# Optimization experiments

Measured on AMD Instinct MI355X. Metric: run time of the kernel, lower is better.

## Reference

```python
import jax, jax.numpy as jnp
import numpy as np

NUM_COMPONENTS = 4
HEADS = 16


def setup_inputs() -> dict:
    key = jax.random.key(0)
    ks = jax.random.split(key, 7)
    BC, S, D = 8, 4096, 1024      # batch_times_comp = batch(2) * num_components(4)
    Se, De = 256, 2048            # encoder seq len, encoder hidden dim
    sc = 0.02                     # keep linear outputs in a sane range
    return {
        "hidden_states": jax.random.normal(ks[0], (BC, S, D), jnp.float32),
        "encoder_hidden_states": jax.random.normal(ks[1], (BC, Se, De), jnp.float32),
        "Wq": jax.random.normal(ks[2], (D, D), jnp.float32) * sc,
        "Wk": jax.random.normal(ks[3], (De, D), jnp.float32) * sc,
        "Wv": jax.random.normal(ks[4], (De, D), jnp.float32) * sc,
        "Wo": jax.random.normal(ks[5], (D, D), jnp.float32) * sc,
        "bo": jnp.zeros((D,), jnp.float32),
    }


def reference(hidden_states, encoder_hidden_states, Wq, Wk, Wv, Wo, bo):
    C, H = NUM_COMPONENTS, HEADS
    BC, S, D = hidden_states.shape
    Se = encoder_hidden_states.shape[1]
    B = BC // C
    dh = D // H
    scale = dh ** -0.5  # attn.scale (learn_temperature=False)

    # projections -> [BC, H, S(e), dh]
    q = (hidden_states @ Wq).reshape(BC, S, H, dh).transpose(0, 2, 1, 3)
    k = (encoder_hidden_states @ Wk).reshape(BC, Se, H, dh).transpose(0, 2, 1, 3)
    v = (encoder_hidden_states @ Wv).reshape(BC, Se, H, dh).transpose(0, 2, 1, 3)

    # dense scores [BC, H, S, Se]
    scores = jnp.einsum("bhsd,bhtd->bhst", q, k) * scale
    # softmax over the COMPONENT axis (dim 0 after the 5D view)
    scores5 = scores.reshape(C, B, H, S, Se)
    w = jax.nn.softmax(scores5, axis=0)  # [C, B, H, S, Se]

    # compositional (negative) entropy, summed over components -> [B, H, S, Se]
    compositional_entropy = (w * jnp.log(w)).sum(axis=0)

    # rescale and attend
    w = (w * (C / Se)).reshape(BC, H, S, Se)
    out = jnp.einsum("bhst,bhtd->bhsd", w, v)
    out = out.transpose(0, 2, 1, 3).reshape(BC, S, D)

    # to_out[0] linear (+bias), to_out[1] dropout = identity at eval,
    # residual connection, rescale_output_factor = 1
    out = out @ Wo + bo + hidden_states
    return out, compositional_entropy
```

## Files before the change

### kernel.cpp

```cpp
#include <hip/hip_runtime.h>

typedef unsigned short u16;
typedef __bf16 bf16x4 __attribute__((ext_vector_type(4)));
typedef __bf16 bf16x8 __attribute__((ext_vector_type(8)));
typedef float f32x4 __attribute__((ext_vector_type(4)));
typedef u16 u16x4 __attribute__((ext_vector_type(4)));
typedef u16 u16x8 __attribute__((ext_vector_type(8)));

#define AS1P(p) ((__attribute__((address_space(1))) void*)(unsigned long long)(p))
#define AS3P(p) ((__attribute__((address_space(3))) void*)(unsigned long long)(p))
#define MFMA16(a, b, c) __builtin_amdgcn_mfma_f32_16x16x32_bf16((a), (b), (c), 0, 0, 0)

__device__ __forceinline__ u16 f2b(float x) { return __builtin_bit_cast(u16, (__bf16)x); }
__device__ __forceinline__ float b2f(u16 u) {
  return __builtin_bit_cast(float, (unsigned)u << 16);
}

__global__ __launch_bounds__(256) void cvt_f32_bf16(const float* __restrict__ in,
                                                    u16* __restrict__ out, int n4) {
  int stride = gridDim.x * blockDim.x;
  for (int i = blockIdx.x * blockDim.x + threadIdx.x; i < n4; i += stride) {
    f32x4 v = *(const f32x4*)(in + (long)i * 4);
    u16x4 o;
    o[0] = f2b(v[0]); o[1] = f2b(v[1]); o[2] = f2b(v[2]); o[3] = f2b(v[3]);
    *(u16x4*)(out + (long)i * 4) = o;
  }
}

__global__ __launch_bounds__(256) void wtrans(const float* __restrict__ W,
                                              u16* __restrict__ Wt, int K, int N) {
  __shared__ float tile[32][33];
  int nbk = K >> 5;
  int bk = blockIdx.x % nbk;
  int bn = blockIdx.x / nbk;
  int tx = threadIdx.x & 31, ty = threadIdx.x >> 5;
#pragma unroll
  for (int i = 0; i < 32; i += 8)
    tile[ty + i][tx] = W[(long)(bk * 32 + ty + i) * N + bn * 32 + tx];
  __syncthreads();
#pragma unroll
  for (int i = 0; i < 32; i += 8)
    Wt[(long)(bn * 32 + ty + i) * K + bk * 32 + tx] = f2b(tile[tx][ty + i]);
}

__global__ __launch_bounds__(256) void vtrans(const u16* __restrict__ kvb,
                                              u16* __restrict__ vt) {
  __shared__ u16 tile[32][33];
  int bt = blockIdx.x & 7;
  int bd = (blockIdx.x >> 3) & 31;
  int bc = blockIdx.x >> 8;
  int tx = threadIdx.x & 31, ty = threadIdx.x >> 5;
  const long ob = (long)bc * 1024 * 256;
  const float RS = 1.0f / 64.0f;
#pragma unroll
  for (int i = 0; i < 32; i += 8)
    tile[ty + i][tx] =
        kvb[((long)bc * 256 + bt * 32 + ty + i) * 2048 + 1024 + bd * 32 + tx];
  __syncthreads();
#pragma unroll
  for (int i = 0; i < 32; i += 8)
    vt[ob + (long)(bd * 32 + ty + i) * 256 + bt * 32 + tx] =
        f2b(b2f(tile[tx][ty + i]) * RS);
}

__global__ __launch_bounds__(256) void kfrag_build(const u16* __restrict__ kvb,
                                                   u16* __restrict__ kfrag) {
  int wv = ((int)blockIdx.x << 2) + (threadIdx.x >> 6);
  int lane = threadIdx.x & 63, lr = lane & 15, lg = lane >> 4;
  int ks = wv & 1, tsl = (wv >> 1) & 1, c = (wv >> 2) & 3;
  int ch = (wv >> 4) & 7, h = (wv >> 7) & 15, b = (wv >> 11) & 1;
  const u16* src = kvb + ((long)(c * 2 + b) * 256 + ch * 32 + tsl * 16 + lr) * 2048 +
                   h * 64 + ks * 32 + lg * 8;
  *(bf16x8*)(kfrag + (long)wv * 512 + lane * 8) = *(const bf16x8*)src;
}

__global__ __launch_bounds__(256) void vfrag_build(const u16* __restrict__ vtb,
                                                   u16* __restrict__ vfrag) {
  int wv = ((int)blockIdx.x << 2) + (threadIdx.x >> 6);
  int lane = threadIdx.x & 63, lr = lane & 15, lg = lane >> 4;
  int dsu = wv & 3, c = (wv >> 2) & 3;
  int ch = (wv >> 4) & 7, h = (wv >> 7) & 15, b = (wv >> 11) & 1;
  const u16* src = vtb + ((long)(c * 2 + b) * 1024 + h * 64 + dsu * 16 + lr) * 256 +
                   ch * 32 + lg * 8;
  *(bf16x8*)(vfrag + (long)wv * 512 + lane * 8) = *(const bf16x8*)src;
}

__global__ __launch_bounds__(256) void gemm_bt(
    const u16* __restrict__ A, const u16* __restrict__ Bt,
    u16* __restrict__ outb, int M, int N, int K, float ascale) {
  __shared__ u16 lA[128 * 64];
  __shared__ u16 lB[128 * 64];
  const int tid = threadIdx.x;
  const int lane = tid & 63;
  const int wid = tid >> 6;
  const int wm = wid >> 1, wn = wid & 1;
  const int lr = lane & 15, lg = lane >> 4;

  int bid = (int)blockIdx.x;
  int nwg = (int)gridDim.x;
  if ((nwg & 7) == 0) bid = (bid & 7) * (nwg >> 3) + (bid >> 3);

  const int nbn = N >> 7;
  const int bm = bid / nbn;
  const int bn = bid % nbn;
  const long arow0 = (long)bm * 128;
  const long brow0 = (long)bn * 128;

  f32x4 acc[4][4] = {};

  const int srow = tid >> 3;
  const int scol = tid & 7;

  for (int k0 = 0; k0 < K; k0 += 64) {
#pragma unroll
    for (int i = 0; i < 4; ++i) {
      int row = i * 32 + srow;
      int kc = scol ^ (row & 7);
      __builtin_amdgcn_global_load_lds(AS1P(A + (arow0 + row) * K + k0 + kc * 8),
                                       AS3P(lA + i * 2048 + (tid & ~63) * 8), 16, 0, 0);
    }
#pragma unroll
    for (int i = 0; i < 4; ++i) {
      int row = i * 32 + srow;
      int kc = scol ^ (row & 7);
      __builtin_amdgcn_global_load_lds(AS1P(Bt + (brow0 + row) * K + k0 + kc * 8),
                                       AS3P(lB + i * 2048 + (tid & ~63) * 8), 16, 0, 0);
    }
    asm volatile("s_waitcnt vmcnt(0)" ::: "memory");
    __syncthreads();

#pragma unroll
    for (int ks = 0; ks < 2; ++ks) {
      bf16x8 af[4], bfr[4];
#pragma unroll
      for (int m = 0; m < 4; ++m) {
        int row = wm * 64 + m * 16 + lr;
        int off = row * 128 + ks * 64 + lg * 16;
        off ^= (row & 7) << 4;
        af[m] = *(const bf16x8*)((const char*)lA + off);
      }
#pragma unroll
      for (int n = 0; n < 4; ++n) {
        int row = wn * 64 + n * 16 + lr;
        int off = row * 128 + ks * 64 + lg * 16;
        off ^= (row & 7) << 4;
        bfr[n] = *(const bf16x8*)((const char*)lB + off);
      }
#pragma unroll
      for (int m = 0; m < 4; ++m)
#pragma unroll
        for (int n = 0; n < 4; ++n)
          acc[m][n] = MFMA16(af[m], bfr[n], acc[m][n]);
    }
    __syncthreads();
  }

#pragma unroll
  for (int m = 0; m < 4; ++m)
#pragma unroll
    for (int n = 0; n < 4; ++n) {
      long col = brow0 + wn * 64 + n * 16 + lr;
#pragma unroll
      for (int r = 0; r < 4; ++r) {
        long row = arow0 + wm * 64 + m * 16 + lg * 4 + r;
        outb[row * N + col] = f2b(acc[m][n][r] * ascale);
      }
    }
}

template <int MODE>
__global__ __launch_bounds__(512, 2) void gemm256(
    const u16* __restrict__ A, const u16* __restrict__ Bt,
    u16* __restrict__ outb, float* __restrict__ outf,
    const float* __restrict__ bias, const u16* __restrict__ residb,
    int M, int N, int K, float ascale) {
  __shared__ u16 lds[2][2][256 * 64];
  const int tid = threadIdx.x;
  const int lane = tid & 63;
  const int wid = tid >> 6;
  const int wm = wid >> 2;
  const int wn = wid & 3;
  const int lr = lane & 15, lg = lane >> 4;

  int bid = (int)blockIdx.x;
  int nwg = (int)gridDim.x;
  bid = (bid & 7) * (nwg >> 3) + (bid >> 3);

  const int nbn = N >> 8;
  const int bm = bid / nbn;
  const int bn = bid % nbn;
  const long arow0 = (long)bm * 256;
  const long brow0 = (long)bn * 256;

  f32x4 acc[8][4] = {};

  const int srow = tid >> 3;
  const int scol = tid & 7;
  const int nt = K >> 6;

#define STAGE256(bf, t)                                                                \
  do {                                                                                 \
    int k0_ = (t) << 6;                                                                \
    _Pragma("unroll") for (int i = 0; i < 4; ++i) {                                    \
      int row = i * 64 + srow;                                                         \
      int kc = scol ^ (row & 7);                                                       \
      __builtin_amdgcn_global_load_lds(AS1P(A + (arow0 + row) * K + k0_ + kc * 8),     \
                                       AS3P(&lds[bf][0][0] + i * 4096 + (tid & ~63) * 8), \
                                       16, 0, 0);                                      \
    }                                                                                  \
    _Pragma("unroll") for (int i = 0; i < 4; ++i) {                                    \
      int row = i * 64 + srow;                                                         \
      int kc = scol ^ (row & 7);                                                       \
      __builtin_amdgcn_global_load_lds(AS1P(Bt + (brow0 + row) * K + k0_ + kc * 8),    \
                                       AS3P(&lds[bf][1][0] + i * 4096 + (tid & ~63) * 8), \
                                       16, 0, 0);                                      \
    }                                                                                  \
  } while (0)

#define COMPUTE256(bf)                                                                 \
  do {                                                                                 \
    _Pragma("unroll") for (int ks = 0; ks < 2; ++ks) {                                 \
      bf16x8 af[8], bfr[4];                                                            \
      _Pragma("unroll") for (int m = 0; m < 8; ++m) {                                  \
        int row = wm * 128 + m * 16 + lr;                                              \
        int off = row * 128 + ks * 64 + lg * 16;                                       \
        off ^= (row & 7) << 4;                                                         \
        af[m] = *(const bf16x8*)((const char*)&lds[bf][0][0] + off);                   \
      }                                                                                \
      _Pragma("unroll") for (int n = 0; n < 4; ++n) {                                  \
        int row = wn * 64 + n * 16 + lr;                                               \
        int off = row * 128 + ks * 64 + lg * 16;                                       \
        off ^= (row & 7) << 4;                                                         \
        bfr[n] = *(const bf16x8*)((const char*)&lds[bf][1][0] + off);                  \
      }                                                                                \
      _Pragma("unroll") for (int m = 0; m < 8; ++m)                                    \
          _Pragma("unroll") for (int n = 0; n < 4; ++n)                                \
              acc[m][n] = MFMA16(af[m], bfr[n], acc[m][n]);                            \
    }                                                                                  \
  } while (0)

  STAGE256(0, 0);
  asm volatile("s_waitcnt vmcnt(0)" ::: "memory");
  __syncthreads();
  int cur = 0;
  for (int t = 0; t < nt - 1; ++t) {
    STAGE256(cur ^ 1, t + 1);
    COMPUTE256(cur);
    asm volatile("s_waitcnt vmcnt(0)" ::: "memory");
    __syncthreads();
    cur ^= 1;
  }
  COMPUTE256(cur);

#pragma unroll
  for (int m = 0; m < 8; ++m)
#pragma unroll
    for (int n = 0; n < 4; ++n) {
      long col = brow0 + wn * 64 + n * 16 + lr;
#pragma unroll
      for (int r = 0; r < 4; ++r) {
        long row = arow0 + wm * 128 + m * 16 + lg * 4 + r;
        float v = acc[m][n][r];
        if (MODE == 1) {
          long idx = row * N + col;
          __builtin_nontemporal_store(v + bias[col] + b2f(residb[idx]), outf + idx);
        } else {
          outb[row * N + col] = f2b(v * ascale);
        }
      }
    }
#undef STAGE256
#undef COMPUTE256
}

__global__ __launch_bounds__(256, 1) void attn_fused(
    const u16* q,
    const u16* __restrict__ kfrag,
    const u16* __restrict__ vfrag,
    u16* attnout,
    float* __restrict__ ent) {
  const int B = 2, H = 16, S = 4096, Se = 256, D = 1024;
  __shared__ u16 ldsP[4 * 2304];
  const int tid = threadIdx.x;
  const int lane = tid & 63, wid = tid >> 6;
  const int lr = lane & 15, lg = lane >> 4;
  int bid = (int)blockIdx.x;
  bid = (bid & 7) * 256 + (bid >> 3);
  const int sblk = bid & 63;
  const int h = (bid >> 6) & 15;
  const int b = bid >> 10;
  const int s0 = sblk * 64 + wid * 16;

  u16* Pw = ldsP + wid * 2304;

  bf16x8 qf[4][2];
#pragma unroll
  for (int c = 0; c < 4; ++c)
#pragma unroll
    for (int ks = 0; ks < 2; ++ks)
      qf[c][ks] = *(const bf16x8*)(q + ((c * B + b) * (long)S + s0 + lr) * D +
                                   h * 64 + ks * 32 + lg * 8);

  const u16* kbh = kfrag + (long)(b * 16 + h) * 65536 + lane * 8;
  const u16* vbh = vfrag + (long)(b * 16 + h) * 65536 + lane * 8;
  float* entp = ent + ((long)(b * H + h) * S + s0 + lg * 4) * Se + lr;

  const float LN2 = 0.69314718056f;

  f32x4 oacc[4][4] = {};

  bf16x8 kf[16];
#pragma unroll
  for (int i = 0; i < 16; ++i) kf[i] = *(const bf16x8*)(kbh + (i << 9));

#pragma unroll
  for (int ch = 0; ch < 8; ++ch) {
    const u16* vc = vbh + ch * 8192;
    bf16x8 vf[16];
#pragma unroll
    for (int i = 0; i < 16; ++i) vf[i] = *(const bf16x8*)(vc + (i << 9));
    bf16x8 kfn[16];
    if (ch < 7) {
      const u16* kn = kbh + (ch + 1) * 8192;
#pragma unroll
      for (int i = 0; i < 16; ++i) kfn[i] = *(const bf16x8*)(kn + (i << 9));
    }
    __builtin_amdgcn_sched_barrier(0);

    f32x4 sacc[4][2] = {};
#pragma unroll
    for (int c = 0; c < 4; ++c)
#pragma unroll
      for (int tsl = 0; tsl < 2; ++tsl)
#pragma unroll
        for (int ks = 0; ks < 2; ++ks)
          sacc[c][tsl] = MFMA16(qf[c][ks], kf[c * 4 + tsl * 2 + ks], sacc[c][tsl]);

#pragma unroll
    for (int tsl = 0; tsl < 2; ++tsl) {
#pragma unroll
      for (int r = 0; r < 4; ++r) {
        float t0 = sacc[0][tsl][r];
        float t1 = sacc[1][tsl][r];
        float t2 = sacc[2][tsl][r];
        float t3 = sacc[3][tsl][r];
        float e0 = __builtin_amdgcn_exp2f(t0);
        float e1 = __builtin_amdgcn_exp2f(t1);
        float e2 = __builtin_amdgcn_exp2f(t2);
        float e3 = __builtin_amdgcn_exp2f(t3);
        float sum = (e0 + e1) + (e2 + e3);
        float inv = __builtin_amdgcn_rcpf(sum);
        float l2s = __builtin_amdgcn_logf(sum);
        float w0 = e0 * inv, w1 = e1 * inv, w2 = e2 * inv, w3 = e3 * inv;
        float entv = (w0 * t0 + w1 * t1 + w2 * t2 + w3 * t3 - l2s) * LN2;
        __builtin_nontemporal_store(entv, entp + r * Se + ch * 32 + tsl * 16);
        int pof = (lg * 4 + r) * 36 + tsl * 16 + lr;
        Pw[0 * 576 + pof] = f2b(w0);
        Pw[1 * 576 + pof] = f2b(w1);
        Pw[2 * 576 + pof] = f2b(w2);
        Pw[3 * 576 + pof] = f2b(w3);
      }
    }

#pragma unroll
    for (int c = 0; c < 4; ++c) {
      union { bf16x4 hh[2]; bf16x8 v; } pu;
      pu.hh[0] = *(const bf16x4*)(Pw + c * 576 + lr * 36 + lg * 8);
      pu.hh[1] = *(const bf16x4*)(Pw + c * 576 + lr * 36 + lg * 8 + 4);
      bf16x8 pf = pu.v;
#pragma unroll
      for (int dsu = 0; dsu < 4; ++dsu)
        oacc[c][dsu] = MFMA16(pf, vf[c * 4 + dsu], oacc[c][dsu]);
    }

    if (ch < 7) {
#pragma unroll
      for (int i = 0; i < 16; ++i) kf[i] = kfn[i];
    }
  }

#pragma unroll
  for (int c = 0; c < 4; ++c)
#pragma unroll
    for (int dsu = 0; dsu < 4; ++dsu)
#pragma unroll
      for (int r = 0; r < 4; ++r) {
        int s = s0 + lg * 4 + r;
        attnout[((c * B + b) * (long)S + s) * D + h * 64 + dsu * 16 + lr] =
            f2b(oacc[c][dsu][r]);
      }
}

extern "C" void kernel_launch(void* const* d_in, const int* in_sizes, int n_in,
                              void* d_out, int out_size, void* d_ws, size_t ws_size,
                              hipStream_t stream) {
  const float* hs  = (const float*)d_in[0];
  const float* ehs = (const float*)d_in[1];
  const float* Wq  = (const float*)d_in[2];
  const float* Wk  = (const float*)d_in[3];
  const float* Wv  = (const float*)d_in[4];
  const float* Wo  = (const float*)d_in[5];
  const float* bo  = (const float*)d_in[6];
  float* out = (float*)d_out;
  float* ent = out + (size_t)8 * 4096 * 1024;

  char* ws = (char*)d_ws;
  u16* hsb   = (u16*)(ws);
  u16* ehsb  = (u16*)(ws + 67108864);
  u16* kfrag = (u16*)(ws + 67108864);
  u16* vfrag = (u16*)(ws + 71303168);
  u16* wqT   = (u16*)(ws + 75497472);
  u16* wkT   = (u16*)(ws + 77594624);
  u16* wvT   = (u16*)(ws + 81788928);
  u16* woT   = (u16*)(ws + 85983232);
  u16* qb    = (u16*)(ws + 88080384);
  u16* kvb   = (u16*)(ws + 155189248);
  u16* vtb   = (u16*)(ws + 163577856);

  const float QSCALE = 0.125f * 1.44269504f;

  cvt_f32_bf16<<<2048, 256, 0, stream>>>(hs, hsb, (8 * 4096 * 1024) / 4);
  cvt_f32_bf16<<<512, 256, 0, stream>>>(ehs, ehsb, (8 * 256 * 2048) / 4);
  wtrans<<<1024, 256, 0, stream>>>(Wq, wqT, 1024, 1024);
  wtrans<<<2048, 256, 0, stream>>>(Wk, wkT, 2048, 1024);
  wtrans<<<2048, 256, 0, stream>>>(Wv, wvT, 2048, 1024);
  wtrans<<<1024, 256, 0, stream>>>(Wo, woT, 1024, 1024);
  gemm256<0><<<(32768 / 256) * (1024 / 256), 512, 0, stream>>>(
      hsb, wqT, qb, nullptr, nullptr, nullptr, 32768, 1024, 1024, QSCALE);
  gemm_bt<<<(2048 / 128) * (2048 / 128), 256, 0, stream>>>(
      ehsb, wkT, kvb, 2048, 2048, 2048, 1.0f);
  vtrans<<<2048, 256, 0, stream>>>(kvb, vtb);
  kfrag_build<<<1024, 256, 0, stream>>>(kvb, kfrag);
  vfrag_build<<<1024, 256, 0, stream>>>(vtb, vfrag);
  attn_fused<<<2048, 256, 0, stream>>>(qb, kfrag, vfrag, qb, ent);
  gemm256<1><<<(32768 / 256) * (1024 / 256), 512, 0, stream>>>(
      qb, woT, nullptr, out, bo, hsb, 32768, 1024, 1024, 1.0f);
}
```

Baseline: 394.7 us.

## Stage K/V fragments in LDS with double buffering and double rows per wave

The attention kernel now stages K and V fragments for each 32-key chunk into a double-buffered LDS region using direct global-to-LDS loads shared by all four waves, instead of each wave loading them into registers from global memory. Each wave also handles 32 query rows instead of 16, so every K/V fragment read from LDS feeds two MFMAs, and the grid is halved. This cuts redundant global K/V traffic and register pressure from the prefetch, at the cost of more LDS, a block barrier per chunk, and fewer blocks in flight.

```diff
diff --git a/kernel.cpp b/kernel.cpp
--- a/kernel.cpp
+++ b/kernel.cpp
@@ -280,103 +280,123 @@
     u16* attnout,
     float* __restrict__ ent) {
   const int B = 2, H = 16, S = 4096, Se = 256, D = 1024;
-  __shared__ u16 ldsP[4 * 2304];
+  __shared__ u16 kvs[2][32 * 512];
+  __shared__ u16 ldsP[4 * 4608];
   const int tid = threadIdx.x;
   const int lane = tid & 63, wid = tid >> 6;
   const int lr = lane & 15, lg = lane >> 4;
   int bid = (int)blockIdx.x;
-  bid = (bid & 7) * 256 + (bid >> 3);
-  const int sblk = bid & 63;
-  const int h = (bid >> 6) & 15;
-  const int b = bid >> 10;
-  const int s0 = sblk * 64 + wid * 16;
-
-  u16* Pw = ldsP + wid * 2304;
-
-  bf16x8 qf[4][2];
+  bid = (bid & 7) * 128 + (bid >> 3);
+  const int sblk = bid & 31;
+  const int h = (bid >> 5) & 15;
+  const int b = bid >> 9;
+  const int s0 = sblk * 128 + wid * 32;
+
+  u16* Pw = ldsP + wid * 4608;
+
+  bf16x8 qf[4][2][2];
 #pragma unroll
   for (int c = 0; c < 4; ++c)
 #pragma unroll
-    for (int ks = 0; ks < 2; ++ks)
-      qf[c][ks] = *(const bf16x8*)(q + ((c * B + b) * (long)S + s0 + lr) * D +
-                                   h * 64 + ks * 32 + lg * 8);
-
-  const u16* kbh = kfrag + (long)(b * 16 + h) * 65536 + lane * 8;
-  const u16* vbh = vfrag + (long)(b * 16 + h) * 65536 + lane * 8;
+    for (int st = 0; st < 2; ++st)
+#pragma unroll
+      for (int ks = 0; ks < 2; ++ks)
+        qf[c][st][ks] =
+            *(const bf16x8*)(q + ((c * B + b) * (long)S + s0 + st * 16 + lr) * D +
+                             h * 64 + ks * 32 + lg * 8);
+
+  const u16* kbh = kfrag + (long)(b * 16 + h) * 65536;
+  const u16* vbh = vfrag + (long)(b * 16 + h) * 65536;
   float* entp = ent + ((long)(b * H + h) * S + s0 + lg * 4) * Se + lr;
 
   const float LN2 = 0.69314718056f;
-
-  f32x4 oacc[4][4] = {};
-
-  bf16x8 kf[16];
-#pragma unroll
-  for (int i = 0; i < 16; ++i) kf[i] = *(const bf16x8*)(kbh + (i << 9));
+  const int g0 = wid * 8;
+
+  f32x4 oacc[4][4][2] = {};
+
+#define STAGEKV(buf, ch)                                                               \
+  do {                                                                                 \
+    _Pragma("unroll") for (int j = 0; j < 8; ++j) {                                    \
+      int f = g0 + j;                                                                  \
+      const u16* src = (f < 16 ? kbh + (ch) * 8192 + f * 512                           \
+                               : vbh + (ch) * 8192 + (f - 16) * 512) +                 \
+                       lane * 8;                                                       \
+      __builtin_amdgcn_global_load_lds(AS1P(src), AS3P(&kvs[buf][f * 512]), 16, 0, 0); \
+    }                                                                                  \
+  } while (0)
+
+  STAGEKV(0, 0);
+  __syncthreads();
 
 #pragma unroll
   for (int ch = 0; ch < 8; ++ch) {
-    const u16* vc = vbh + ch * 8192;
-    bf16x8 vf[16];
-#pragma unroll
-    for (int i = 0; i < 16; ++i) vf[i] = *(const bf16x8*)(vc + (i << 9));
-    bf16x8 kfn[16];
-    if (ch < 7) {
-      const u16* kn = kbh + (ch + 1) * 8192;
-#pragma unroll
-      for (int i = 0; i < 16; ++i) kfn[i] = *(const bf16x8*)(kn + (i << 9));
-    }
-    __builtin_amdgcn_sched_barrier(0);
-
-    f32x4 sacc[4][2] = {};
+    const int cur = ch & 1;
+    if (ch < 7) STAGEKV(cur ^ 1, ch + 1);
+    const u16* KV = kvs[cur];
+
+    f32x4 sacc[2][4][2] = {};
 #pragma unroll
     for (int c = 0; c < 4; ++c)
 #pragma unroll
       for (int tsl = 0; tsl < 2; ++tsl)
 #pragma unroll
-        for (int ks = 0; ks < 2; ++ks)
-          sacc[c][tsl] = MFMA16(qf[c][ks], kf[c * 4 + tsl * 2 + ks], sacc[c][tsl]);
-
-#pragma unroll
-    for (int tsl = 0; tsl < 2; ++tsl) {
-#pragma unroll
-      for (int r = 0; r < 4; ++r) {
-        float t0 = sacc[0][tsl][r];
-        float t1 = sacc[1][tsl][r];
-        float t2 = sacc[2][tsl][r];
-        float t3 = sacc[3][tsl][r];
-        float e0 = __builtin_amdgcn_exp2f(t0);
-        float e1 = __builtin_amdgcn_exp2f(t1);
-        float e2 = __builtin_amdgcn_exp2f(t2);
-        float e3 = __builtin_amdgcn_exp2f(t3);
-        float sum = (e0 + e1) + (e2 + e3);
-        float inv = __builtin_amdgcn_rcpf(sum);
-        float l2s = __builtin_amdgcn_logf(sum);
-        float w0 = e0 * inv, w1 = e1 * inv, w2 = e2 * inv, w3 = e3 * inv;
-        float entv = (w0 * t0 + w1 * t1 + w2 * t2 + w3 * t3 - l2s) * LN2;
-        __builtin_nontemporal_store(entv, entp + r * Se + ch * 32 + tsl * 16);
-        int pof = (lg * 4 + r) * 36 + tsl * 16 + lr;
-        Pw[0 * 576 + pof] = f2b(w0);
-        Pw[1 * 576 + pof] = f2b(w1);
-        Pw[2 * 576 + pof] = f2b(w2);
-        Pw[3 * 576 + pof] = f2b(w3);
+        for (int ks = 0; ks < 2; ++ks) {
+          bf16x8 kfv = *(const bf16x8*)(KV + (c * 4 + tsl * 2 + ks) * 512 + lane * 8);
+#pragma unroll
+          for (int st = 0; st < 2; ++st)
+            sacc[st][c][tsl] = MFMA16(qf[c][st][ks], kfv, sacc[st][c][tsl]);
+        }
+
+#pragma unroll
+    for (int st = 0; st < 2; ++st) {
+#pragma unroll
+      for (int tsl = 0; tsl < 2; ++tsl) {
+#pragma unroll
+        for (int r = 0; r < 4; ++r) {
+          float t0 = sacc[st][0][tsl][r];
+          float t1 = sacc[st][1][tsl][r];
+          float t2 = sacc[st][2][tsl][r];
+          float t3 = sacc[st][3][tsl][r];
+          float e0 = __builtin_amdgcn_exp2f(t0);
+          float e1 = __builtin_amdgcn_exp2f(t1);
+          float e2 = __builtin_amdgcn_exp2f(t2);
+          float e3 = __builtin_amdgcn_exp2f(t3);
+          float sum = (e0 + e1) + (e2 + e3);
+          float inv = __builtin_amdgcn_rcpf(sum);
+          float l2s = __builtin_amdgcn_logf(sum);
+          float w0 = e0 * inv, w1 = e1 * inv, w2 = e2 * inv, w3 = e3 * inv;
+          float entv = (w0 * t0 + w1 * t1 + w2 * t2 + w3 * t3 - l2s) * LN2;
+          __builtin_nontemporal_store(
+              entv, entp + (st * 16 + r) * Se + ch * 32 + tsl * 16);
+          int prow = st * 16 + lg * 4 + r;
+          int pof = prow * 36 + tsl * 16 + lr;
+          Pw[0 * 1152 + pof] = f2b(w0);
+          Pw[1 * 1152 + pof] = f2b(w1);
+          Pw[2 * 1152 + pof] = f2b(w2);
+          Pw[3 * 1152 + pof] = f2b(w3);
+        }
       }
     }
 
 #pragma unroll
     for (int c = 0; c < 4; ++c) {
-      union { bf16x4 hh[2]; bf16x8 v; } pu;
-      pu.hh[0] = *(const bf16x4*)(Pw + c * 576 + lr * 36 + lg * 8);
-      pu.hh[1] = *(const bf16x4*)(Pw + c * 576 + lr * 36 + lg * 8 + 4);
-      bf16x8 pf = pu.v;
-#pragma unroll
-      for (int dsu = 0; dsu < 4; ++dsu)
-        oacc[c][dsu] = MFMA16(pf, vf[c * 4 + dsu], oacc[c][dsu]);
-    }
-
-    if (ch < 7) {
-#pragma unroll
-      for (int i = 0; i < 16; ++i) kf[i] = kfn[i];
-    }
+      bf16x8 pf[2];
+#pragma unroll
+      for (int st = 0; st < 2; ++st) {
+        union { bf16x4 hh[2]; bf16x8 v; } pu;
+        pu.hh[0] = *(const bf16x4*)(Pw + c * 1152 + (st * 16 + lr) * 36 + lg * 8);
+        pu.hh[1] = *(const bf16x4*)(Pw + c * 1152 + (st * 16 + lr) * 36 + lg * 8 + 4);
+        pf[st] = pu.v;
+      }
+#pragma unroll
+      for (int dsu = 0; dsu < 4; ++dsu) {
+        bf16x8 vfv = *(const bf16x8*)(KV + (16 + c * 4 + dsu) * 512 + lane * 8);
+        oacc[c][dsu][0] = MFMA16(pf[0], vfv, oacc[c][dsu][0]);
+        oacc[c][dsu][1] = MFMA16(pf[1], vfv, oacc[c][dsu][1]);
+      }
+    }
+
+    __syncthreads();
   }
 
 #pragma unroll
@@ -384,11 +404,14 @@
 #pragma unroll
     for (int dsu = 0; dsu < 4; ++dsu)
 #pragma unroll
-      for (int r = 0; r < 4; ++r) {
-        int s = s0 + lg * 4 + r;
-        attnout[((c * B + b) * (long)S + s) * D + h * 64 + dsu * 16 + lr] =
-            f2b(oacc[c][dsu][r]);
-      }
+      for (int st = 0; st < 2; ++st)
+#pragma unroll
+        for (int r = 0; r < 4; ++r) {
+          long s = s0 + st * 16 + lg * 4 + r;
+          attnout[((c * B + b) * (long)S + s) * D + h * 64 + dsu * 16 + lr] =
+              f2b(oacc[c][dsu][st][r]);
+        }
+#undef STAGEKV
 }
 
 extern "C" void kernel_launch(void* const* d_in, const int* in_sizes, int n_in,
@@ -432,7 +455,7 @@
   vtrans<<<2048, 256, 0, stream>>>(kvb, vtb);
   kfrag_build<<<1024, 256, 0, stream>>>(kvb, kfrag);
   vfrag_build<<<1024, 256, 0, stream>>>(vtb, vfrag);
-  attn_fused<<<2048, 256, 0, stream>>>(qb, kfrag, vfrag, qb, ent);
+  attn_fused<<<1024, 256, 0, stream>>>(qb, kfrag, vfrag, qb, ent);
   gemm256<1><<<(32768 / 256) * (1024 / 256), 512, 0, stream>>>(
       qb, woT, nullptr, out, bo, hsb, 32768, 1024, 1024, 1.0f);
 }
```

Result: faster. 371.2 us, median of 2 (-6.0%).
